# Kernel optimization log

Measured on AMD Instinct MI355X. Metric: run time of the kernel, lower is better.

## Reference

```python
import jax, jax.numpy as jnp
import numpy as np

NUM_LABELS = 1024
NUM_CAMS = 8


def setup_inputs() -> dict:
    key = jax.random.key(0)
    k1, k2, k3 = jax.random.split(key, 3)
    feats = jax.random.normal(k1, (16384, 2048), dtype=jnp.float32)
    labels = jax.random.randint(k2, (16384,), 0, NUM_LABELS, dtype=jnp.int64)
    cam_ids = jax.random.randint(k3, (16384,), 0, NUM_CAMS, dtype=jnp.int64)
    return {"feats": feats, "labels": labels, "cam_ids": cam_ids}


def reference(feats, labels, cam_ids):
    # Combined (person-id, camera-id) segment id -> fused segment-mean.
    seg = labels * NUM_CAMS + cam_ids  # [N]
    num_segments = NUM_LABELS * NUM_CAMS
    sums = jax.ops.segment_sum(feats, seg, num_segments=num_segments)  # [S, D]
    counts = jax.ops.segment_sum(jnp.ones_like(seg, dtype=feats.dtype), seg,
                                 num_segments=num_segments)  # [S]
    means = sums / jnp.maximum(counts, 1.0)[:, None]
    # targets[i] = mean of feats over group(label_i, cam_i); detached in torch.
    targets = jax.lax.stop_gradient(means[seg])  # [N, D]
    # SmoothL1 (beta=1), reduction='mean'
    d = feats - targets
    ad = jnp.abs(d)
    loss = jnp.mean(jnp.where(ad < 1.0, 0.5 * d * d, ad - 0.5))
    return loss
```

## Files before the change

### kernel.cpp

```cpp
#include <hip/hip_runtime.h>
#include <hip/hip_bf16.h>

#define N_ROWS 16384
#define D_COLS 2048
#define NUM_LABELS 1024
#define NUM_CAMS 8
#define NUM_SEG (NUM_LABELS * NUM_CAMS)
#define MAXPER 64

__global__ void build_lists_kernel(const int* __restrict__ labels,
                                   const int* __restrict__ cams,
                                   int* __restrict__ counts,
                                   int* __restrict__ lists) {
    int i = blockIdx.x * blockDim.x + threadIdx.x;
    if (i < N_ROWS) {
        int seg = labels[i] * NUM_CAMS + cams[i];
        int pos = atomicAdd(&counts[seg], 1);
        if (pos < MAXPER) lists[seg * MAXPER + pos] = i;
    }
}

__device__ __forceinline__ float smooth_l1(float d) {
    float ad = fabsf(d);
    return ad < 1.0f ? 0.5f * d * d : ad - 0.5f;
}

__global__ __launch_bounds__(256) void seg_loss_kernel(const float* __restrict__ feats,
                                                       const int* __restrict__ counts,
                                                       const int* __restrict__ lists,
                                                       float* __restrict__ loss_acc) {
    int seg = blockIdx.x;
    int tid = threadIdx.x;
    int cnt = counts[seg];
    float local = 0.0f;

    if (cnt > 0) {
        int rows = cnt < MAXPER ? cnt : MAXPER;
        const int* lst = lists + seg * MAXPER;

        float m0x = 0.f, m0y = 0.f, m0z = 0.f, m0w = 0.f;
        float m1x = 0.f, m1y = 0.f, m1z = 0.f, m1w = 0.f;

        for (int r = 0; r < rows; ++r) {
            int row = lst[r];
            const float4* rp = (const float4*)(feats + (size_t)row * D_COLS);
            float4 a = rp[tid];
            float4 b = rp[tid + 256];
            m0x += a.x; m0y += a.y; m0z += a.z; m0w += a.w;
            m1x += b.x; m1y += b.y; m1z += b.z; m1w += b.w;
        }
        float inv = 1.0f / (float)cnt;
        m0x *= inv; m0y *= inv; m0z *= inv; m0w *= inv;
        m1x *= inv; m1y *= inv; m1z *= inv; m1w *= inv;

        for (int r = 0; r < rows; ++r) {
            int row = lst[r];
            const float4* rp = (const float4*)(feats + (size_t)row * D_COLS);
            float4 a = rp[tid];
            float4 b = rp[tid + 256];
            local += smooth_l1(a.x - m0x) + smooth_l1(a.y - m0y)
                   + smooth_l1(a.z - m0z) + smooth_l1(a.w - m0w);
            local += smooth_l1(b.x - m1x) + smooth_l1(b.y - m1y)
                   + smooth_l1(b.z - m1z) + smooth_l1(b.w - m1w);
        }
    }

    for (int off = 32; off > 0; off >>= 1)
        local += __shfl_down(local, off, 64);

    __shared__ float wsum[4];
    int lane = tid & 63;
    int wid  = tid >> 6;
    if (lane == 0) wsum[wid] = local;
    __syncthreads();
    if (tid == 0) {
        float s = wsum[0] + wsum[1] + wsum[2] + wsum[3];
        if (s != 0.0f) atomicAdd(loss_acc, s);
    }
}

__global__ void finalize_kernel(const float* __restrict__ loss_acc, float* __restrict__ out) {
    out[0] = loss_acc[0] * (1.0f / ((float)N_ROWS * (float)D_COLS));
}

extern "C" void kernel_launch(void* const* d_in, const int* in_sizes, int n_in,
                              void* d_out, int out_size, void* d_ws, size_t ws_size,
                              hipStream_t stream) {
    const float* feats = (const float*)d_in[0];
    const int* labels  = (const int*)d_in[1];
    const int* cams    = (const int*)d_in[2];
    float* out = (float*)d_out;

    int* counts = (int*)d_ws;
    float* acc  = (float*)(counts + NUM_SEG);
    int* lists  = (int*)(acc + 1);

    hipMemsetAsync(d_ws, 0, (NUM_SEG + 1) * sizeof(int), stream);

    build_lists_kernel<<<(N_ROWS + 255) / 256, 256, 0, stream>>>(labels, cams, counts, lists);
    seg_loss_kernel<<<NUM_SEG, 256, 0, stream>>>(feats, counts, lists, acc);
    finalize_kernel<<<1, 1, 0, stream>>>(acc, out);
}
```

Baseline: 231.0 us.

## Cache segment rows in registers, split columns across two blocks, drop finalize kernel

The segment loss kernel now loads up to 16 rows of the segment into registers once and reuses them for both the mean and the SmoothL1 pass. This avoids re-reading feats from memory in the second pass. Each segment is split across two blocks by column half, doubling the grid and halving per-thread work. The finalize kernel is removed by scaling inside the atomicAdd and zeroing the output with a memset. The cost is higher register pressure from the 16 float4 buffers, which may lower occupancy.

```diff
diff --git a/kernel.cpp b/kernel.cpp
--- a/kernel.cpp
+++ b/kernel.cpp
@@ -7,6 +7,8 @@
 #define NUM_CAMS 8
 #define NUM_SEG (NUM_LABELS * NUM_CAMS)
 #define MAXPER 64
+#define R_REG 16
+#define F4_PER_ROW (D_COLS / 4)
 
 __global__ void build_lists_kernel(const int* __restrict__ labels,
                                    const int* __restrict__ cams,
@@ -28,45 +30,60 @@
 __global__ __launch_bounds__(256) void seg_loss_kernel(const float* __restrict__ feats,
                                                        const int* __restrict__ counts,
                                                        const int* __restrict__ lists,
-                                                       float* __restrict__ loss_acc) {
-    int seg = blockIdx.x;
-    int tid = threadIdx.x;
-    int cnt = counts[seg];
+                                                       float* __restrict__ out) {
+    int seg  = blockIdx.x >> 1;
+    int half = blockIdx.x & 1;
+    int tid  = threadIdx.x;
+    int cnt  = counts[seg];
     float local = 0.0f;
 
     if (cnt > 0) {
         int rows = cnt < MAXPER ? cnt : MAXPER;
         const int* lst = lists + seg * MAXPER;
+        int off = half * 256 + tid;
+        const float4* base = (const float4*)feats;
 
-        float m0x = 0.f, m0y = 0.f, m0z = 0.f, m0w = 0.f;
-        float m1x = 0.f, m1y = 0.f, m1z = 0.f, m1w = 0.f;
+        int idx[R_REG];
+#pragma unroll
+        for (int r = 0; r < R_REG; ++r)
+            idx[r] = (r < rows) ? lst[r] : -1;
 
-        for (int r = 0; r < rows; ++r) {
-            int row = lst[r];
-            const float4* rp = (const float4*)(feats + (size_t)row * D_COLS);
-            float4 a = rp[tid];
-            float4 b = rp[tid + 256];
-            m0x += a.x; m0y += a.y; m0z += a.z; m0w += a.w;
-            m1x += b.x; m1y += b.y; m1z += b.z; m1w += b.w;
+        float4 v[R_REG];
+#pragma unroll
+        for (int r = 0; r < R_REG; ++r) {
+            v[r] = make_float4(0.f, 0.f, 0.f, 0.f);
+            if (idx[r] >= 0)
+                v[r] = base[(size_t)idx[r] * F4_PER_ROW + off];
+        }
+
+        float mx = 0.f, my = 0.f, mz = 0.f, mw = 0.f;
+#pragma unroll
+        for (int r = 0; r < R_REG; ++r) {
+            mx += v[r].x; my += v[r].y; mz += v[r].z; mw += v[r].w;
+        }
+        for (int r = R_REG; r < rows; ++r) {
+            float4 a = base[(size_t)lst[r] * F4_PER_ROW + off];
+            mx += a.x; my += a.y; mz += a.z; mw += a.w;
         }
         float inv = 1.0f / (float)cnt;
-        m0x *= inv; m0y *= inv; m0z *= inv; m0w *= inv;
-        m1x *= inv; m1y *= inv; m1z *= inv; m1w *= inv;
+        mx *= inv; my *= inv; mz *= inv; mw *= inv;
 
-        for (int r = 0; r < rows; ++r) {
-            int row = lst[r];
-            const float4* rp = (const float4*)(feats + (size_t)row * D_COLS);
-            float4 a = rp[tid];
-            float4 b = rp[tid + 256];
-            local += smooth_l1(a.x - m0x) + smooth_l1(a.y - m0y)
-                   + smooth_l1(a.z - m0z) + smooth_l1(a.w - m0w);
-            local += smooth_l1(b.x - m1x) + smooth_l1(b.y - m1y)
-                   + smooth_l1(b.z - m1z) + smooth_l1(b.w - m1w);
+#pragma unroll
+        for (int r = 0; r < R_REG; ++r) {
+            if (idx[r] >= 0) {
+                local += smooth_l1(v[r].x - mx) + smooth_l1(v[r].y - my)
+                       + smooth_l1(v[r].z - mz) + smooth_l1(v[r].w - mw);
+            }
+        }
+        for (int r = R_REG; r < rows; ++r) {
+            float4 a = base[(size_t)lst[r] * F4_PER_ROW + off];
+            local += smooth_l1(a.x - mx) + smooth_l1(a.y - my)
+                   + smooth_l1(a.z - mz) + smooth_l1(a.w - mw);
         }
     }
 
-    for (int off = 32; off > 0; off >>= 1)
-        local += __shfl_down(local, off, 64);
+    for (int o = 32; o > 0; o >>= 1)
+        local += __shfl_down(local, o, 64);
 
     __shared__ float wsum[4];
     int lane = tid & 63;
@@ -75,12 +92,9 @@
     __syncthreads();
     if (tid == 0) {
         float s = wsum[0] + wsum[1] + wsum[2] + wsum[3];
-        if (s != 0.0f) atomicAdd(loss_acc, s);
+        if (s != 0.0f)
+            atomicAdd(out, s * (1.0f / ((float)N_ROWS * (float)D_COLS)));
     }
-}
-
-__global__ void finalize_kernel(const float* __restrict__ loss_acc, float* __restrict__ out) {
-    out[0] = loss_acc[0] * (1.0f / ((float)N_ROWS * (float)D_COLS));
 }
 
 extern "C" void kernel_launch(void* const* d_in, const int* in_sizes, int n_in,
@@ -92,12 +106,11 @@
     float* out = (float*)d_out;
 
     int* counts = (int*)d_ws;
-    float* acc  = (float*)(counts + NUM_SEG);
-    int* lists  = (int*)(acc + 1);
+    int* lists  = counts + NUM_SEG;
 
-    hipMemsetAsync(d_ws, 0, (NUM_SEG + 1) * sizeof(int), stream);
+    hipMemsetAsync(counts, 0, NUM_SEG * sizeof(int), stream);
+    hipMemsetAsync(out, 0, sizeof(float), stream);
 
     build_lists_kernel<<<(N_ROWS + 255) / 256, 256, 0, stream>>>(labels, cams, counts, lists);
-    seg_loss_kernel<<<NUM_SEG, 256, 0, stream>>>(feats, counts, lists, acc);
-    finalize_kernel<<<1, 1, 0, stream>>>(acc, out);
+    seg_loss_kernel<<<NUM_SEG * 2, 256, 0, stream>>>(feats, counts, lists, out);
 }
```

After: 277.5 us. 20.1% more time.
